# Optimization experiments

Hardware: AMD Instinct MI355X
Metric: run time of the kernel (lower is better)

The kernel has to match this reference:

```python
import jax, jax.numpy as jnp
import numpy as np

B, C1, C2, K, S, P, D, HDIM, BINS = 4, 32, 64, 3, 1, 1, 1, 64, 16
H = W = 96

def _unfold(x):
    # torch F.unfold: (B, C*k*k, L) with channel-major (c, kh, kw) ordering,
    # which matches conv_general_dilated_patches' output feature ordering.
    p = jax.lax.conv_general_dilated_patches(
        x, filter_shape=(K, K), window_strides=(S, S),
        padding=((P, P), (P, P)), rhs_dilation=(D, D))  # (B, C*k*k, Ho, Wo)
    b, ckk, ho, wo = p.shape
    return p.reshape(b, ckk, ho * wo), ho, wo

def _patch_stats(patches):
    # patches: (B, Ckk, L); stop-gradient stats [mu, sigma, gamma, kappa, entropy]
    b, ckk, L = patches.shape
    mu = patches.mean(axis=1, keepdims=True)
    diff = patches - mu
    var = (diff * diff).mean(axis=1, keepdims=True)
    sigma = jnp.sqrt(var + 1e-6)
    z = diff / (sigma + 1e-6)
    gamma = (z ** 3).mean(axis=1, keepdims=True)
    kappa = (z ** 4).mean(axis=1, keepdims=True) - 3.0
    p_min = patches.min(axis=1, keepdims=True)
    p_max = patches.max(axis=1, keepdims=True)
    p_norm = (patches - p_min) / (p_max - p_min + 1e-6)
    bin_idx = jnp.clip((p_norm * (BINS - 1)).astype(jnp.int32), 0, BINS - 1)
    # histogram via flat scatter-add: counts[b, bin, l]
    b_ix = jnp.arange(b, dtype=jnp.int32)[:, None, None]
    l_ix = jnp.arange(L, dtype=jnp.int32)[None, None, :]
    flat = ((b_ix * BINS + bin_idx) * L + l_ix).ravel()
    counts = jnp.zeros(b * BINS * L, dtype=patches.dtype).at[flat].add(1.0)
    counts = counts.reshape(b, BINS, L)
    prob = counts / (ckk + 1e-6)
    entropy = -(prob * jnp.log(prob + 1e-9)).sum(axis=1, keepdims=True)
    stats = jnp.concatenate([mu, sigma, gamma, kappa, entropy], axis=1)  # (B,5,L)
    return jax.lax.stop_gradient(stats)

def setup_inputs() -> dict:
    key = jax.random.key(0)
    ks = jax.random.split(key, 8)
    x = jax.random.normal(ks[0], (B, C1, H, W), dtype=jnp.float32)
    fc1_w = jax.random.normal(ks[1], (HDIM, 5), dtype=jnp.float32) / np.sqrt(5.0)
    fc1_b = jax.random.normal(ks[2], (HDIM,), dtype=jnp.float32) * 0.01
    alpha_w = jax.random.normal(ks[3], (C2, HDIM), dtype=jnp.float32) * 0.01
    alpha_b = jnp.ones((C2,), dtype=jnp.float32)
    phi_w = jax.random.normal(ks[4], (C1 * K * K, HDIM), dtype=jnp.float32) * 0.01
    phi_b = jnp.zeros((C1 * K * K,), dtype=jnp.float32)
    bn_gamma = jnp.ones((C2,), dtype=jnp.float32)
    bn_beta = jnp.zeros((C2,), dtype=jnp.float32)
    bn_mean = jax.random.normal(ks[5], (C2,), dtype=jnp.float32) * 0.1
    bn_var = jax.random.uniform(ks[6], (C2,), dtype=jnp.float32, minval=0.5, maxval=1.5)
    return {"x": x, "fc1_w": fc1_w, "fc1_b": fc1_b, "alpha_w": alpha_w,
            "alpha_b": alpha_b, "phi_w": phi_w, "phi_b": phi_b,
            "bn_gamma": bn_gamma, "bn_beta": bn_beta,
            "bn_mean": bn_mean, "bn_var": bn_var}

def reference(x, fc1_w, fc1_b, alpha_w, alpha_b, phi_w, phi_b,
              bn_gamma, bn_beta, bn_mean, bn_var):
    patches, ho, wo = _unfold(x)           # (B, C1*K*K, L)
    b, ckk, L = patches.shape
    stats = _patch_stats(patches)          # (B, 5, L), stop-grad
    s = stats.transpose(0, 2, 1).reshape(b * L, 5)
    h = jax.nn.relu(s @ fc1_w.T + fc1_b)                 # (B*L, HDIM)
    alpha = (h @ alpha_w.T + alpha_b).reshape(b, L, C2)  # (B, L, C2)
    phi = (h @ phi_w.T + phi_b).reshape(b, L, ckk)       # (B, L, Ckk)
    # kernel = alpha[:,None] * phi[None,:]; out = kernel @ patch
    # == alpha * (phi . patch), computed without materializing kernels
    proj = jnp.einsum('blj,bjl->bl', phi, patches)       # (B, L)
    out = alpha * proj[:, :, None]                       # (B, L, C2)
    out = out.transpose(0, 2, 1).reshape(b, C2, ho, wo)
    # BatchNorm2d (eval: running stats) + SiLU
    inv = bn_gamma / jnp.sqrt(bn_var + 1e-5)
    y = (out - bn_mean[None, :, None, None]) * inv[None, :, None, None] \
        + bn_beta[None, :, None, None]
    return jax.nn.silu(y)
```

## Files before the change

### kernel.cpp

```cpp
#include <hip/hip_runtime.h>

#define FLT_MAX_ 3.402823466e+38f

constexpr int PARTS = 8;
constexpr int CB    = 4;
constexpr int HW    = 9216;
constexpr int AOFF  = 4608;

using bf16x8 = __attribute__((ext_vector_type(8))) short;
using f32x4  = __attribute__((ext_vector_type(4))) float;
using u32x4  = __attribute__((ext_vector_type(4))) unsigned int;

__device__ inline unsigned cvtpk_bf16(float a, float b) {
    unsigned r;
    asm("v_cvt_pk_bf16_f32 %0, %1, %2" : "=v"(r) : "v"(a), "v"(b));
    return r;
}
__device__ inline void split2(float p0, float p1, unsigned &h, unsigned &l) {
    h = cvtpk_bf16(p0, p1);
    const float h0 = __builtin_bit_cast(float, h << 16);
    const float h1 = __builtin_bit_cast(float, h & 0xFFFF0000u);
    l = cvtpk_bf16(p0 - h0, p1 - h1);
}

__global__ __launch_bounds__(256)
void prep_w(const float* __restrict__ phi_w, const float* __restrict__ alpha_w,
            u32x4* __restrict__ wsq) {
    const int kb   = blockIdx.x;
    const int n    = threadIdx.x >> 6;
    const int lane = threadIdx.x & 63;
    const int lg   = lane >> 4, kk = lane & 15;
    if (kb < 9) {
        float p[8];
        #pragma unroll
        for (int jj = 0; jj < 8; ++jj) {
            const int ch = lg * 8 + jj;
            p[jj] = phi_w[(ch * 9 + kb) * 64 + n * 16 + kk];
        }
        unsigned h0,h1,h2,h3, l0,l1,l2,l3;
        split2(p[0],p[1],h0,l0); split2(p[2],p[3],h1,l1);
        split2(p[4],p[5],h2,l2); split2(p[6],p[7],h3,l3);
        wsq[(kb * 4 + n) * 64 + lane]        = u32x4{h0,h1,h2,h3};
        wsq[2304 + (kb * 4 + n) * 64 + lane] = u32x4{l0,l1,l2,l3};
    } else {
        #pragma unroll
        for (int kblk = 0; kblk < 2; ++kblk) {
            float p[8];
            #pragma unroll
            for (int jj = 0; jj < 8; ++jj) {
                const int k = kblk * 32 + lg * 8 + jj;
                p[jj] = alpha_w[(n * 16 + kk) * 64 + k];
            }
            unsigned h0,h1,h2,h3, l0,l1,l2,l3;
            split2(p[0],p[1],h0,l0); split2(p[2],p[3],h1,l1);
            split2(p[4],p[5],h2,l2); split2(p[6],p[7],h3,l3);
            wsq[AOFF + (kblk * 4 + n) * 64 + lane]       = u32x4{h0,h1,h2,h3};
            wsq[AOFF + 512 + (kblk * 4 + n) * 64 + lane] = u32x4{l0,l1,l2,l3};
        }
    }
}

__global__ __launch_bounds__(512, 3)
void sac_fused(const float* __restrict__ x,
               const float* __restrict__ fc1_w, const float* __restrict__ fc1_b,
               const float* __restrict__ alpha_b,
               const float* __restrict__ phi_b,
               const float* __restrict__ bn_g, const float* __restrict__ bn_b,
               const float* __restrict__ bn_m, const float* __restrict__ bn_v,
               const u32x4* __restrict__ wsq,
               float* __restrict__ out)
{
    __shared__ float    h_lds[64 * 65];
    __shared__ float    red7[7 * 512];
    __shared__ unsigned cnts[16 * 64];

    const int tid  = threadIdx.x;
    const int lane = tid & 63;
    const int w    = __builtin_amdgcn_readfirstlane(tid >> 6);
    const int g    = blockIdx.x;
    const int b    = g / 144;
    const int rem  = g - b * 144;
    const int ty   = rem / 3;
    const int tx   = rem - ty * 3;
    const int y0   = ty * 2, x0 = tx * 32;
    const int r    = lane >> 5;
    const int c    = lane & 31;
    const int row  = y0 + r, col = x0 + c;

    cnts[tid] = 0u;
    cnts[tid + 512] = 0u;

    const float* __restrict__ xb = x + (size_t)b * 32 * HW;
    const float* __restrict__ xw = xb + (size_t)(w * CB) * HW;

    float pv[36];
    float s1 = 0.f, s2 = 0.f, s3 = 0.f, s4 = 0.f;
    float mn = FLT_MAX_, mx = -FLT_MAX_, projp = 0.f;
    #pragma unroll
    for (int dy = 0; dy < 3; ++dy) {
        const int y    = row + dy - 1;
        const bool yok = (unsigned)y < 96u;
        #pragma unroll
        for (int dx = 0; dx < 3; ++dx) {
            const int xx2 = col + dx - 1;
            const bool ok = yok && ((unsigned)xx2 < 96u);
            const int off = y * 96 + xx2;
            #pragma unroll
            for (int cc = 0; cc < CB; ++cc) {
                const float p = ok ? xw[cc * HW + off] : 0.f;
                pv[(dy * 3 + dx) * 4 + cc] = p;
                const float pp = p * p;
                s1 += p;
                s2 = fmaf(p, p, s2);
                s3 = fmaf(pp, p, s3);
                s4 = fmaf(pp, pp, s4);
                mn = fminf(mn, p);
                mx = fmaxf(mx, p);
                const int j = (w * CB + cc) * 9 + dy * 3 + dx;
                projp = fmaf(p, phi_b[j], projp);
            }
        }
    }
    red7[tid]         = s1;
    red7[512 + tid]   = mn;
    red7[1024 + tid]  = mx;
    red7[1536 + tid]  = s2;
    red7[2048 + tid]  = s3;
    red7[2560 + tid]  = s4;
    red7[3072 + tid]  = projp;
    __syncthreads();

    float ts1 = 0.f, tmn = FLT_MAX_, tmx = -FLT_MAX_;
    #pragma unroll
    for (int rr = 0; rr < PARTS; ++rr) {
        ts1 += red7[rr * 64 + lane];
        tmn = fminf(tmn, red7[512 + rr * 64 + lane]);
        tmx = fmaxf(tmx, red7[1024 + rr * 64 + lane]);
    }
    const float mu   = ts1 * (1.0f / 288.0f);
    const float rng  = (tmx - tmn) + 1e-6f;
    const float invr = 1.0f / rng;

    #pragma unroll
    for (int i = 0; i < 36; ++i) {
        const float pn = (pv[i] - tmn) * invr;
        int bi = (int)(pn * 15.0f);
        bi = bi < 0 ? 0 : (bi > 15 ? 15 : bi);
        atomicAdd(&cnts[bi * 64 + lane], 1u);
    }
    __syncthreads();

    {
        float u2 = 0.f, u3 = 0.f, u4 = 0.f;
        #pragma unroll
        for (int rr = 0; rr < PARTS; ++rr) {
            u2 += red7[1536 + rr * 64 + lane];
            u3 += red7[2048 + rr * 64 + lane];
            u4 += red7[2560 + rr * 64 + lane];
        }
        const float e2  = u2 * (1.0f / 288.0f);
        const float e3  = u3 * (1.0f / 288.0f);
        const float e4  = u4 * (1.0f / 288.0f);
        const float mu2 = mu * mu;
        const float var = fmaxf(e2 - mu2, 0.f);
        const float m3  = e3 - 3.f * mu * e2 + 2.f * mu * mu2;
        const float m4  = e4 - 4.f * mu * e3 + 6.f * mu2 * e2 - 3.f * mu2 * mu2;
        const float sig = sqrtf(var + 1e-6f);
        const float inv = 1.0f / (sig + 1e-6f);
        const float inv2 = inv * inv;
        const float gam = m3 * (inv2 * inv);
        const float kap = m4 * (inv2 * inv2) - 3.0f;
        float ent = 0.f;
        #pragma unroll
        for (int bi = 0; bi < 16; ++bi) {
            const float prob = (float)cnts[bi * 64 + lane] * (1.0f / 288.0f);
            ent -= prob * __logf(prob + 1e-9f);
        }
        #pragma unroll
        for (int kk = 0; kk < 8; ++kk) {
            const int k = w * 8 + kk;
            float acc = fc1_b[k];
            acc = fmaf(mu,  fc1_w[k * 5 + 0], acc);
            acc = fmaf(sig, fc1_w[k * 5 + 1], acc);
            acc = fmaf(gam, fc1_w[k * 5 + 2], acc);
            acc = fmaf(kap, fc1_w[k * 5 + 3], acc);
            acc = fmaf(ent, fc1_w[k * 5 + 4], acc);
            h_lds[lane * 65 + k] = fmaxf(acc, 0.f);
        }
    }
    __syncthreads();

    const int m    = w >> 1;
    const int np   = (w & 1) * 2;
    const int lg   = lane >> 4;

    {
        const int posa = m * 16 + (lane & 15);
        const int ra   = posa >> 5, ca = posa & 31;
        const int rowa = y0 + ra, cola = x0 + ca;
        const float* __restrict__ xg8 = xb + (size_t)(lg * 8) * HW;

        f32x4 acc0 = {0.f, 0.f, 0.f, 0.f};
        f32x4 acc1 = {0.f, 0.f, 0.f, 0.f};

        #pragma unroll
        for (int tap = 0; tap < 9; ++tap) {
            const int dy = tap / 3, dx = tap % 3;
            const u32x4 bh0 = wsq[(tap * 4 + np) * 64 + lane];
            const u32x4 bh1 = wsq[(tap * 4 + np + 1) * 64 + lane];
            const u32x4 bl0 = wsq[2304 + (tap * 4 + np) * 64 + lane];
            const u32x4 bl1 = wsq[2304 + (tap * 4 + np + 1) * 64 + lane];

            const int ya = rowa + dy - 1, xa = cola + dx - 1;
            const bool ok = ((unsigned)ya < 96u) && ((unsigned)xa < 96u);
            const int off = ya * 96 + xa;
            const float p0 = ok ? xg8[0 * HW + off] : 0.f;
            const float p1 = ok ? xg8[1 * HW + off] : 0.f;
            const float p2 = ok ? xg8[2 * HW + off] : 0.f;
            const float p3 = ok ? xg8[3 * HW + off] : 0.f;
            const float p4 = ok ? xg8[4 * HW + off] : 0.f;
            const float p5 = ok ? xg8[5 * HW + off] : 0.f;
            const float p6 = ok ? xg8[6 * HW + off] : 0.f;
            const float p7 = ok ? xg8[7 * HW + off] : 0.f;
            unsigned ah0,ah1,ah2,ah3, al0,al1,al2,al3;
            split2(p0,p1,ah0,al0); split2(p2,p3,ah1,al1);
            split2(p4,p5,ah2,al2); split2(p6,p7,ah3,al3);
            const bf16x8 Ah  = __builtin_bit_cast(bf16x8, u32x4{ah0,ah1,ah2,ah3});
            const bf16x8 Al  = __builtin_bit_cast(bf16x8, u32x4{al0,al1,al2,al3});
            const bf16x8 Bh0 = __builtin_bit_cast(bf16x8, bh0);
            const bf16x8 Bl0 = __builtin_bit_cast(bf16x8, bl0);
            const bf16x8 Bh1 = __builtin_bit_cast(bf16x8, bh1);
            const bf16x8 Bl1 = __builtin_bit_cast(bf16x8, bl1);

            acc0 = __builtin_amdgcn_mfma_f32_16x16x32_bf16(Ah, Bh0, acc0, 0, 0, 0);
            acc0 = __builtin_amdgcn_mfma_f32_16x16x32_bf16(Ah, Bl0, acc0, 0, 0, 0);
            acc0 = __builtin_amdgcn_mfma_f32_16x16x32_bf16(Al, Bh0, acc0, 0, 0, 0);
            acc1 = __builtin_amdgcn_mfma_f32_16x16x32_bf16(Ah, Bh1, acc1, 0, 0, 0);
            acc1 = __builtin_amdgcn_mfma_f32_16x16x32_bf16(Ah, Bl1, acc1, 0, 0, 0);
            acc1 = __builtin_amdgcn_mfma_f32_16x16x32_bf16(Al, Bh1, acc1, 0, 0, 0);
        }

        const int k0 = np * 16 + (lane & 15);
        const int k1 = k0 + 16;
        float pr0, pr1, pr2, pr3;
        {
            const int pb = (m * 16 + lg * 4) * 65;
            pr0 = acc0[0] * h_lds[pb + 0 * 65 + k0] + acc1[0] * h_lds[pb + 0 * 65 + k1];
            pr1 = acc0[1] * h_lds[pb + 1 * 65 + k0] + acc1[1] * h_lds[pb + 1 * 65 + k1];
            pr2 = acc0[2] * h_lds[pb + 2 * 65 + k0] + acc1[2] * h_lds[pb + 2 * 65 + k1];
            pr3 = acc0[3] * h_lds[pb + 3 * 65 + k0] + acc1[3] * h_lds[pb + 3 * 65 + k1];
        }
        #pragma unroll
        for (int msk = 1; msk < 16; msk <<= 1) {
            pr0 += __shfl_xor(pr0, msk);
            pr1 += __shfl_xor(pr1, msk);
            pr2 += __shfl_xor(pr2, msk);
            pr3 += __shfl_xor(pr3, msk);
        }
        if ((lane & 15) == 0) {
            const int pb = m * 16 + lg * 4;
            red7[(pb + 0) * 2 + (w & 1)] = pr0;
            red7[(pb + 1) * 2 + (w & 1)] = pr1;
            red7[(pb + 2) * 2 + (w & 1)] = pr2;
            red7[(pb + 3) * 2 + (w & 1)] = pr3;
        }
    }
    __syncthreads();

    const int pb4 = m * 16 + lg * 4;
    float pj0, pj1, pj2, pj3;
    {
        const f32x4 rp0 = *(const f32x4*)&red7[2 * pb4];
        const f32x4 rp1 = *(const f32x4*)&red7[2 * pb4 + 4];
        pj0 = rp0[0] + rp0[1];
        pj1 = rp0[2] + rp0[3];
        pj2 = rp1[0] + rp1[1];
        pj3 = rp1[2] + rp1[3];
        #pragma unroll
        for (int rr = 0; rr < PARTS; ++rr) {
            const f32x4 ph = *(const f32x4*)&red7[3072 + rr * 64 + pb4];
            pj0 += ph[0]; pj1 += ph[1]; pj2 += ph[2]; pj3 += ph[3];
        }
    }

    f32x4 ac0 = {0.f, 0.f, 0.f, 0.f};
    f32x4 ac1 = {0.f, 0.f, 0.f, 0.f};
    #pragma unroll
    for (int kblk = 0; kblk < 2; ++kblk) {
        const float* hp = &h_lds[(m * 16 + (lane & 15)) * 65 + kblk * 32 + lg * 8];
        const float h0 = hp[0], h1 = hp[1], h2 = hp[2], h3 = hp[3];
        const float h4 = hp[4], h5 = hp[5], h6 = hp[6], h7 = hp[7];
        unsigned ah0,ah1,ah2,ah3, al0,al1,al2,al3;
        split2(h0,h1,ah0,al0); split2(h2,h3,ah1,al1);
        split2(h4,h5,ah2,al2); split2(h6,h7,ah3,al3);
        const bf16x8 Ah = __builtin_bit_cast(bf16x8, u32x4{ah0,ah1,ah2,ah3});
        const bf16x8 Al = __builtin_bit_cast(bf16x8, u32x4{al0,al1,al2,al3});
        const u32x4 bh0 = wsq[AOFF + (kblk * 4 + np) * 64 + lane];
        const u32x4 bh1 = wsq[AOFF + (kblk * 4 + np + 1) * 64 + lane];
        const u32x4 bl0 = wsq[AOFF + 512 + (kblk * 4 + np) * 64 + lane];
        const u32x4 bl1 = wsq[AOFF + 512 + (kblk * 4 + np + 1) * 64 + lane];
        const bf16x8 Bh0 = __builtin_bit_cast(bf16x8, bh0);
        const bf16x8 Bl0 = __builtin_bit_cast(bf16x8, bl0);
        const bf16x8 Bh1 = __builtin_bit_cast(bf16x8, bh1);
        const bf16x8 Bl1 = __builtin_bit_cast(bf16x8, bl1);
        ac0 = __builtin_amdgcn_mfma_f32_16x16x32_bf16(Ah, Bh0, ac0, 0, 0, 0);
        ac0 = __builtin_amdgcn_mfma_f32_16x16x32_bf16(Ah, Bl0, ac0, 0, 0, 0);
        ac0 = __builtin_amdgcn_mfma_f32_16x16x32_bf16(Al, Bh0, ac0, 0, 0, 0);
        ac1 = __builtin_amdgcn_mfma_f32_16x16x32_bf16(Ah, Bh1, ac1, 0, 0, 0);
        ac1 = __builtin_amdgcn_mfma_f32_16x16x32_bf16(Ah, Bl1, ac1, 0, 0, 0);
        ac1 = __builtin_amdgcn_mfma_f32_16x16x32_bf16(Al, Bh1, ac1, 0, 0, 0);
    }

    const int c0 = np * 16 + (lane & 15);
    const int r2 = m >> 1;
    const size_t obase = (size_t)(b * 64) * HW
                       + (size_t)(y0 + r2) * 96 + x0 + (m & 1) * 16 + lg * 4;
    {
        const int ch     = c0;
        const float ab_  = alpha_b[ch];
        const float binv = bn_g[ch] * rsqrtf(bn_v[ch] + 1e-5f);
        const float bm_  = bn_m[ch], bb_ = bn_b[ch];
        f32x4 sv;
        {
            const float a0 = ac0[0] + ab_, a1 = ac0[1] + ab_;
            const float a2 = ac0[2] + ab_, a3 = ac0[3] + ab_;
            const float o0 = a0 * pj0, o1 = a1 * pj1, o2 = a2 * pj2, o3 = a3 * pj3;
            const float y0v = (o0 - bm_) * binv + bb_;
            const float y1v = (o1 - bm_) * binv + bb_;
            const float y2v = (o2 - bm_) * binv + bb_;
            const float y3v = (o3 - bm_) * binv + bb_;
            sv[0] = __fdividef(y0v, 1.0f + __expf(-y0v));
            sv[1] = __fdividef(y1v, 1.0f + __expf(-y1v));
            sv[2] = __fdividef(y2v, 1.0f + __expf(-y2v));
            sv[3] = __fdividef(y3v, 1.0f + __expf(-y3v));
        }
        *(f32x4*)&out[obase + (size_t)ch * HW] = sv;
    }
    {
        const int ch     = c0 + 16;
        const float ab_  = alpha_b[ch];
        const float binv = bn_g[ch] * rsqrtf(bn_v[ch] + 1e-5f);
        const float bm_  = bn_m[ch], bb_ = bn_b[ch];
        f32x4 sv;
        {
            const float a0 = ac1[0] + ab_, a1 = ac1[1] + ab_;
            const float a2 = ac1[2] + ab_, a3 = ac1[3] + ab_;
            const float o0 = a0 * pj0, o1 = a1 * pj1, o2 = a2 * pj2, o3 = a3 * pj3;
            const float y0v = (o0 - bm_) * binv + bb_;
            const float y1v = (o1 - bm_) * binv + bb_;
            const float y2v = (o2 - bm_) * binv + bb_;
            const float y3v = (o3 - bm_) * binv + bb_;
            sv[0] = __fdividef(y0v, 1.0f + __expf(-y0v));
            sv[1] = __fdividef(y1v, 1.0f + __expf(-y1v));
            sv[2] = __fdividef(y2v, 1.0f + __expf(-y2v));
            sv[3] = __fdividef(y3v, 1.0f + __expf(-y3v));
        }
        *(f32x4*)&out[obase + (size_t)ch * HW] = sv;
    }
}

extern "C" void kernel_launch(void* const* d_in, const int* in_sizes, int n_in,
                              void* d_out, int out_size, void* d_ws, size_t ws_size,
                              hipStream_t stream) {
    const float* x   = (const float*)d_in[0];
    const float* f1w = (const float*)d_in[1];
    const float* f1b = (const float*)d_in[2];
    const float* aw  = (const float*)d_in[3];
    const float* ab  = (const float*)d_in[4];
    const float* pw  = (const float*)d_in[5];
    const float* pb  = (const float*)d_in[6];
    const float* bg  = (const float*)d_in[7];
    const float* bb  = (const float*)d_in[8];
    const float* bm  = (const float*)d_in[9];
    const float* bv  = (const float*)d_in[10];

    u32x4* wsq = (u32x4*)d_ws;

    prep_w<<<dim3(10), dim3(256), 0, stream>>>(pw, aw, wsq);
    sac_fused<<<dim3(576), dim3(512), 0, stream>>>(
        x, f1w, f1b, ab, pb, bg, bb, bm, bv, wsq, (float*)d_out);
}
```

Baseline: 34.23 us.

## Halve block tile to one row of 32 pixels and reduce stats with wave shuffles

Each block now covers one row of 32 output pixels using 256 threads, so the grid doubles to 1152 blocks. Within a wave, 8 lanes map to pixels and 8 channel groups per pixel, which lets the per-patch moments, min/max and phi-bias projection be reduced with xor shuffles instead of an LDS buffer and a block barrier. The histogram is handled per wave with waitcnt fences in place of __syncthreads. This cuts LDS traffic and barriers and may raise occupancy, but neighbouring blocks now reload more overlapping halo rows.

```diff
diff --git a/kernel.cpp b/kernel.cpp
--- a/kernel.cpp
+++ b/kernel.cpp
@@ -2,10 +2,8 @@
 
 #define FLT_MAX_ 3.402823466e+38f
 
-constexpr int PARTS = 8;
-constexpr int CB    = 4;
-constexpr int HW    = 9216;
-constexpr int AOFF  = 4608;
+constexpr int HW   = 9216;
+constexpr int AOFF = 4608;
 
 using bf16x8 = __attribute__((ext_vector_type(8))) short;
 using f32x4  = __attribute__((ext_vector_type(4))) float;
@@ -60,7 +58,7 @@
     }
 }
 
-__global__ __launch_bounds__(512, 3)
+__global__ __launch_bounds__(256, 6)
 void sac_fused(const float* __restrict__ x,
                const float* __restrict__ fc1_w, const float* __restrict__ fc1_b,
                const float* __restrict__ alpha_b,
@@ -70,97 +68,98 @@
                const u32x4* __restrict__ wsq,
                float* __restrict__ out)
 {
-    __shared__ float    h_lds[64 * 65];
-    __shared__ float    red7[7 * 512];
-    __shared__ unsigned cnts[16 * 64];
+    __shared__ float    h_lds[32 * 65];
+    __shared__ unsigned cnts[16 * 33];
+    __shared__ float    phib[32];
+    __shared__ float    redP[64];
 
     const int tid  = threadIdx.x;
     const int lane = tid & 63;
     const int w    = __builtin_amdgcn_readfirstlane(tid >> 6);
     const int g    = blockIdx.x;
-    const int b    = g / 144;
-    const int rem  = g - b * 144;
-    const int ty   = rem / 3;
-    const int tx   = rem - ty * 3;
-    const int y0   = ty * 2, x0 = tx * 32;
-    const int r    = lane >> 5;
-    const int c    = lane & 31;
-    const int row  = y0 + r, col = x0 + c;
-
-    cnts[tid] = 0u;
-    cnts[tid + 512] = 0u;
+    const int b    = g / 288;
+    const int rem  = g - b * 288;
+    const int y0   = rem / 3;
+    const int x0   = (rem - y0 * 3) * 32;
+
+    const int p8  = lane & 7;
+    const int cg  = lane >> 3;
+    const int pos = w * 8 + p8;
+    const int col = x0 + pos;
 
     const float* __restrict__ xb = x + (size_t)b * 32 * HW;
-    const float* __restrict__ xw = xb + (size_t)(w * CB) * HW;
 
     float pv[36];
     float s1 = 0.f, s2 = 0.f, s3 = 0.f, s4 = 0.f;
-    float mn = FLT_MAX_, mx = -FLT_MAX_, projp = 0.f;
-    #pragma unroll
-    for (int dy = 0; dy < 3; ++dy) {
-        const int y    = row + dy - 1;
-        const bool yok = (unsigned)y < 96u;
-        #pragma unroll
-        for (int dx = 0; dx < 3; ++dx) {
-            const int xx2 = col + dx - 1;
-            const bool ok = yok && ((unsigned)xx2 < 96u);
-            const int off = y * 96 + xx2;
+    float mn = FLT_MAX_, mx = -FLT_MAX_, pj = 0.f;
+    {
+        const float* __restrict__ xc = xb + (size_t)(cg * 4) * HW;
+        #pragma unroll
+        for (int cc = 0; cc < 4; ++cc) {
+            const float* __restrict__ xcc = xc + (size_t)cc * HW;
+            const float* __restrict__ pbp = phi_b + (cg * 4 + cc) * 9;
             #pragma unroll
-            for (int cc = 0; cc < CB; ++cc) {
-                const float p = ok ? xw[cc * HW + off] : 0.f;
-                pv[(dy * 3 + dx) * 4 + cc] = p;
-                const float pp = p * p;
-                s1 += p;
-                s2 = fmaf(p, p, s2);
-                s3 = fmaf(pp, p, s3);
-                s4 = fmaf(pp, pp, s4);
-                mn = fminf(mn, p);
-                mx = fmaxf(mx, p);
-                const int j = (w * CB + cc) * 9 + dy * 3 + dx;
-                projp = fmaf(p, phi_b[j], projp);
+            for (int dy = 0; dy < 3; ++dy) {
+                const int y    = y0 + dy - 1;
+                const bool yok = (unsigned)y < 96u;
+                #pragma unroll
+                for (int dx = 0; dx < 3; ++dx) {
+                    const int xx  = col + dx - 1;
+                    const bool ok = yok && ((unsigned)xx < 96u);
+                    const float p = ok ? xcc[y * 96 + xx] : 0.f;
+                    pv[cc * 9 + dy * 3 + dx] = p;
+                    const float pp = p * p;
+                    s1 += p;
+                    s2 = fmaf(p, p, s2);
+                    s3 = fmaf(pp, p, s3);
+                    s4 = fmaf(pp, pp, s4);
+                    mn = fminf(mn, p);
+                    mx = fmaxf(mx, p);
+                    pj = fmaf(p, pbp[dy * 3 + dx], pj);
+                }
             }
         }
     }
-    red7[tid]         = s1;
-    red7[512 + tid]   = mn;
-    red7[1024 + tid]  = mx;
-    red7[1536 + tid]  = s2;
-    red7[2048 + tid]  = s3;
-    red7[2560 + tid]  = s4;
-    red7[3072 + tid]  = projp;
-    __syncthreads();
-
-    float ts1 = 0.f, tmn = FLT_MAX_, tmx = -FLT_MAX_;
-    #pragma unroll
-    for (int rr = 0; rr < PARTS; ++rr) {
-        ts1 += red7[rr * 64 + lane];
-        tmn = fminf(tmn, red7[512 + rr * 64 + lane]);
-        tmx = fmaxf(tmx, red7[1024 + rr * 64 + lane]);
-    }
-    const float mu   = ts1 * (1.0f / 288.0f);
-    const float rng  = (tmx - tmn) + 1e-6f;
+    #pragma unroll
+    for (int msk = 8; msk < 64; msk <<= 1) {
+        s1 += __shfl_xor(s1, msk);
+        s2 += __shfl_xor(s2, msk);
+        s3 += __shfl_xor(s3, msk);
+        s4 += __shfl_xor(s4, msk);
+        mn = fminf(mn, __shfl_xor(mn, msk));
+        mx = fmaxf(mx, __shfl_xor(mx, msk));
+        pj += __shfl_xor(pj, msk);
+    }
+    if (cg == 0) phib[pos] = pj;
+
+    const float mu   = s1 * (1.0f / 288.0f);
+    const float rng  = (mx - mn) + 1e-6f;
     const float invr = 1.0f / rng;
 
+    cnts[(cg * 2 + 0) * 33 + pos] = 0u;
+    cnts[(cg * 2 + 1) * 33 + pos] = 0u;
+    asm volatile("s_waitcnt lgkmcnt(0)" ::: "memory");
     #pragma unroll
     for (int i = 0; i < 36; ++i) {
-        const float pn = (pv[i] - tmn) * invr;
+        const float pn = (pv[i] - mn) * invr;
         int bi = (int)(pn * 15.0f);
         bi = bi < 0 ? 0 : (bi > 15 ? 15 : bi);
-        atomicAdd(&cnts[bi * 64 + lane], 1u);
-    }
-    __syncthreads();
-
-    {
-        float u2 = 0.f, u3 = 0.f, u4 = 0.f;
-        #pragma unroll
-        for (int rr = 0; rr < PARTS; ++rr) {
-            u2 += red7[1536 + rr * 64 + lane];
-            u3 += red7[2048 + rr * 64 + lane];
-            u4 += red7[2560 + rr * 64 + lane];
-        }
-        const float e2  = u2 * (1.0f / 288.0f);
-        const float e3  = u3 * (1.0f / 288.0f);
-        const float e4  = u4 * (1.0f / 288.0f);
+        atomicAdd(&cnts[bi * 33 + pos], 1u);
+    }
+    asm volatile("s_waitcnt lgkmcnt(0)" ::: "memory");
+    float ent = 0.f;
+    #pragma unroll
+    for (int e = 0; e < 2; ++e) {
+        const float prob = (float)cnts[(cg * 2 + e) * 33 + pos] * (1.0f / 288.0f);
+        ent -= prob * __logf(prob + 1e-9f);
+    }
+    #pragma unroll
+    for (int msk = 8; msk < 64; msk <<= 1) ent += __shfl_xor(ent, msk);
+
+    {
+        const float e2  = s2 * (1.0f / 288.0f);
+        const float e3  = s3 * (1.0f / 288.0f);
+        const float e4  = s4 * (1.0f / 288.0f);
         const float mu2 = mu * mu;
         const float var = fmaxf(e2 - mu2, 0.f);
         const float m3  = e3 - 3.f * mu * e2 + 2.f * mu * mu2;
@@ -170,34 +169,27 @@
         const float inv2 = inv * inv;
         const float gam = m3 * (inv2 * inv);
         const float kap = m4 * (inv2 * inv2) - 3.0f;
-        float ent = 0.f;
-        #pragma unroll
-        for (int bi = 0; bi < 16; ++bi) {
-            const float prob = (float)cnts[bi * 64 + lane] * (1.0f / 288.0f);
-            ent -= prob * __logf(prob + 1e-9f);
-        }
         #pragma unroll
         for (int kk = 0; kk < 8; ++kk) {
-            const int k = w * 8 + kk;
+            const int k = cg * 8 + kk;
             float acc = fc1_b[k];
             acc = fmaf(mu,  fc1_w[k * 5 + 0], acc);
             acc = fmaf(sig, fc1_w[k * 5 + 1], acc);
             acc = fmaf(gam, fc1_w[k * 5 + 2], acc);
             acc = fmaf(kap, fc1_w[k * 5 + 3], acc);
             acc = fmaf(ent, fc1_w[k * 5 + 4], acc);
-            h_lds[lane * 65 + k] = fmaxf(acc, 0.f);
+            h_lds[pos * 65 + k] = fmaxf(acc, 0.f);
         }
     }
     __syncthreads();
 
-    const int m    = w >> 1;
-    const int np   = (w & 1) * 2;
-    const int lg   = lane >> 4;
+    const int m  = w >> 1;
+    const int np = (w & 1) * 2;
+    const int lg = lane >> 4;
 
     {
         const int posa = m * 16 + (lane & 15);
-        const int ra   = posa >> 5, ca = posa & 31;
-        const int rowa = y0 + ra, cola = x0 + ca;
+        const int cola = x0 + posa;
         const float* __restrict__ xg8 = xb + (size_t)(lg * 8) * HW;
 
         f32x4 acc0 = {0.f, 0.f, 0.f, 0.f};
@@ -211,7 +203,7 @@
             const u32x4 bl0 = wsq[2304 + (tap * 4 + np) * 64 + lane];
             const u32x4 bl1 = wsq[2304 + (tap * 4 + np + 1) * 64 + lane];
 
-            const int ya = rowa + dy - 1, xa = cola + dx - 1;
+            const int ya = y0 + dy - 1, xa = cola + dx - 1;
             const bool ok = ((unsigned)ya < 96u) && ((unsigned)xa < 96u);
             const int off = ya * 96 + xa;
             const float p0 = ok ? xg8[0 * HW + off] : 0.f;
@@ -242,14 +234,11 @@
 
         const int k0 = np * 16 + (lane & 15);
         const int k1 = k0 + 16;
-        float pr0, pr1, pr2, pr3;
-        {
-            const int pb = (m * 16 + lg * 4) * 65;
-            pr0 = acc0[0] * h_lds[pb + 0 * 65 + k0] + acc1[0] * h_lds[pb + 0 * 65 + k1];
-            pr1 = acc0[1] * h_lds[pb + 1 * 65 + k0] + acc1[1] * h_lds[pb + 1 * 65 + k1];
-            pr2 = acc0[2] * h_lds[pb + 2 * 65 + k0] + acc1[2] * h_lds[pb + 2 * 65 + k1];
-            pr3 = acc0[3] * h_lds[pb + 3 * 65 + k0] + acc1[3] * h_lds[pb + 3 * 65 + k1];
-        }
+        const int pbr = (m * 16 + lg * 4) * 65;
+        float pr0 = acc0[0] * h_lds[pbr + 0 * 65 + k0] + acc1[0] * h_lds[pbr + 0 * 65 + k1];
+        float pr1 = acc0[1] * h_lds[pbr + 1 * 65 + k0] + acc1[1] * h_lds[pbr + 1 * 65 + k1];
+        float pr2 = acc0[2] * h_lds[pbr + 2 * 65 + k0] + acc1[2] * h_lds[pbr + 2 * 65 + k1];
+        float pr3 = acc0[3] * h_lds[pbr + 3 * 65 + k0] + acc1[3] * h_lds[pbr + 3 * 65 + k1];
         #pragma unroll
         for (int msk = 1; msk < 16; msk <<= 1) {
             pr0 += __shfl_xor(pr0, msk);
@@ -259,29 +248,19 @@
         }
         if ((lane & 15) == 0) {
             const int pb = m * 16 + lg * 4;
-            red7[(pb + 0) * 2 + (w & 1)] = pr0;
-            red7[(pb + 1) * 2 + (w & 1)] = pr1;
-            red7[(pb + 2) * 2 + (w & 1)] = pr2;
-            red7[(pb + 3) * 2 + (w & 1)] = pr3;
+            redP[(pb + 0) * 2 + (w & 1)] = pr0;
+            redP[(pb + 1) * 2 + (w & 1)] = pr1;
+            redP[(pb + 2) * 2 + (w & 1)] = pr2;
+            redP[(pb + 3) * 2 + (w & 1)] = pr3;
         }
     }
     __syncthreads();
 
     const int pb4 = m * 16 + lg * 4;
-    float pj0, pj1, pj2, pj3;
-    {
-        const f32x4 rp0 = *(const f32x4*)&red7[2 * pb4];
-        const f32x4 rp1 = *(const f32x4*)&red7[2 * pb4 + 4];
-        pj0 = rp0[0] + rp0[1];
-        pj1 = rp0[2] + rp0[3];
-        pj2 = rp1[0] + rp1[1];
-        pj3 = rp1[2] + rp1[3];
-        #pragma unroll
-        for (int rr = 0; rr < PARTS; ++rr) {
-            const f32x4 ph = *(const f32x4*)&red7[3072 + rr * 64 + pb4];
-            pj0 += ph[0]; pj1 += ph[1]; pj2 += ph[2]; pj3 += ph[3];
-        }
-    }
+    const float pj0 = redP[(pb4 + 0) * 2] + redP[(pb4 + 0) * 2 + 1] + phib[pb4 + 0];
+    const float pj1 = redP[(pb4 + 1) * 2] + redP[(pb4 + 1) * 2 + 1] + phib[pb4 + 1];
+    const float pj2 = redP[(pb4 + 2) * 2] + redP[(pb4 + 2) * 2 + 1] + phib[pb4 + 2];
+    const float pj3 = redP[(pb4 + 3) * 2] + redP[(pb4 + 3) * 2 + 1] + phib[pb4 + 3];
 
     f32x4 ac0 = {0.f, 0.f, 0.f, 0.f};
     f32x4 ac1 = {0.f, 0.f, 0.f, 0.f};
@@ -312,28 +291,23 @@
     }
 
     const int c0 = np * 16 + (lane & 15);
-    const int r2 = m >> 1;
-    const size_t obase = (size_t)(b * 64) * HW
-                       + (size_t)(y0 + r2) * 96 + x0 + (m & 1) * 16 + lg * 4;
+    const size_t obase = (size_t)(b * 64) * HW + (size_t)y0 * 96 + x0 + m * 16 + lg * 4;
     {
         const int ch     = c0;
         const float ab_  = alpha_b[ch];
         const float binv = bn_g[ch] * rsqrtf(bn_v[ch] + 1e-5f);
         const float bm_  = bn_m[ch], bb_ = bn_b[ch];
+        const float o0 = (ac0[0] + ab_) * pj0, o1 = (ac0[1] + ab_) * pj1;
+        const float o2 = (ac0[2] + ab_) * pj2, o3 = (ac0[3] + ab_) * pj3;
+        const float y0v = (o0 - bm_) * binv + bb_;
+        const float y1v = (o1 - bm_) * binv + bb_;
+        const float y2v = (o2 - bm_) * binv + bb_;
+        const float y3v = (o3 - bm_) * binv + bb_;
         f32x4 sv;
-        {
-            const float a0 = ac0[0] + ab_, a1 = ac0[1] + ab_;
-            const float a2 = ac0[2] + ab_, a3 = ac0[3] + ab_;
-            const float o0 = a0 * pj0, o1 = a1 * pj1, o2 = a2 * pj2, o3 = a3 * pj3;
-            const float y0v = (o0 - bm_) * binv + bb_;
-            const float y1v = (o1 - bm_) * binv + bb_;
-            const float y2v = (o2 - bm_) * binv + bb_;
-            const float y3v = (o3 - bm_) * binv + bb_;
-            sv[0] = __fdividef(y0v, 1.0f + __expf(-y0v));
-            sv[1] = __fdividef(y1v, 1.0f + __expf(-y1v));
-            sv[2] = __fdividef(y2v, 1.0f + __expf(-y2v));
-            sv[3] = __fdividef(y3v, 1.0f + __expf(-y3v));
-        }
+        sv[0] = __fdividef(y0v, 1.0f + __expf(-y0v));
+        sv[1] = __fdividef(y1v, 1.0f + __expf(-y1v));
+        sv[2] = __fdividef(y2v, 1.0f + __expf(-y2v));
+        sv[3] = __fdividef(y3v, 1.0f + __expf(-y3v));
         *(f32x4*)&out[obase + (size_t)ch * HW] = sv;
     }
     {
@@ -341,20 +315,17 @@
         const float ab_  = alpha_b[ch];
         const float binv = bn_g[ch] * rsqrtf(bn_v[ch] + 1e-5f);
         const float bm_  = bn_m[ch], bb_ = bn_b[ch];
+        const float o0 = (ac1[0] + ab_) * pj0, o1 = (ac1[1] + ab_) * pj1;
+        const float o2 = (ac1[2] + ab_) * pj2, o3 = (ac1[3] + ab_) * pj3;
+        const float y0v = (o0 - bm_) * binv + bb_;
+        const float y1v = (o1 - bm_) * binv + bb_;
+        const float y2v = (o2 - bm_) * binv + bb_;
+        const float y3v = (o3 - bm_) * binv + bb_;
         f32x4 sv;
-        {
-            const float a0 = ac1[0] + ab_, a1 = ac1[1] + ab_;
-            const float a2 = ac1[2] + ab_, a3 = ac1[3] + ab_;
-            const float o0 = a0 * pj0, o1 = a1 * pj1, o2 = a2 * pj2, o3 = a3 * pj3;
-            const float y0v = (o0 - bm_) * binv + bb_;
-            const float y1v = (o1 - bm_) * binv + bb_;
-            const float y2v = (o2 - bm_) * binv + bb_;
-            const float y3v = (o3 - bm_) * binv + bb_;
-            sv[0] = __fdividef(y0v, 1.0f + __expf(-y0v));
-            sv[1] = __fdividef(y1v, 1.0f + __expf(-y1v));
-            sv[2] = __fdividef(y2v, 1.0f + __expf(-y2v));
-            sv[3] = __fdividef(y3v, 1.0f + __expf(-y3v));
-        }
+        sv[0] = __fdividef(y0v, 1.0f + __expf(-y0v));
+        sv[1] = __fdividef(y1v, 1.0f + __expf(-y1v));
+        sv[2] = __fdividef(y2v, 1.0f + __expf(-y2v));
+        sv[3] = __fdividef(y3v, 1.0f + __expf(-y3v));
         *(f32x4*)&out[obase + (size_t)ch * HW] = sv;
     }
 }
@@ -377,6 +348,6 @@
     u32x4* wsq = (u32x4*)d_ws;
 
     prep_w<<<dim3(10), dim3(256), 0, stream>>>(pw, aw, wsq);
-    sac_fused<<<dim3(576), dim3(512), 0, stream>>>(
+    sac_fused<<<dim3(1152), dim3(256), 0, stream>>>(
         x, f1w, f1b, ab, pb, bg, bb, bm, bv, wsq, (float*)d_out);
 }
```

Result: slower. 35.70 us (+4.3%).
